# Optimization experiments

Hardware: AMD Instinct MI355X
Metric: run time of the kernel (lower is better)

The kernel has to match this reference:

```python
import jax, jax.numpy as jnp
import numpy as np
import math

N_STATE = 64
H_MODEL = 1024
D_CONV = 16
EXPAND = 2
D_INNER = EXPAND * H_MODEL            # 2048
HEADDIM = H_MODEL // 4                # 256
NHEADS = D_INNER // HEADDIM           # 8
NGROUPS = 1
CONV_DIM = D_INNER + 2 * NGROUPS * N_STATE           # 2176
D_IN_PROJ = 2 * D_INNER + 2 * NGROUPS * N_STATE + NHEADS
BATCH, SEQLEN = 4, 2048


def setup_inputs() -> dict:
    key = jax.random.key(0)
    ks = jax.random.split(key, 10)
    x = jax.random.normal(ks[0], (BATCH, SEQLEN, H_MODEL), jnp.float32)
    W_in = jax.random.normal(ks[1], (H_MODEL, D_IN_PROJ), jnp.float32) * (H_MODEL ** -0.5)
    conv_w = jax.random.normal(ks[2], (CONV_DIM, D_CONV), jnp.float32) * (D_CONV ** -0.5)
    conv_b = jnp.zeros((CONV_DIM,), jnp.float32)
    # inverse-softplus of dt0 in [1e-3, 1e-1] (mamba2 dt init)
    dt0 = jnp.exp(jax.random.uniform(ks[3], (NHEADS,), minval=math.log(1e-3), maxval=math.log(1e-1)))
    dt_bias = jnp.log(jnp.expm1(dt0))
    A_log = jnp.log(jax.random.uniform(ks[4], (NHEADS,), minval=1.0, maxval=16.0))
    D = jnp.ones((NHEADS,), jnp.float32)
    init_states = jax.random.normal(ks[5], (NHEADS, HEADDIM, N_STATE), jnp.float32) * 0.01
    norm_w = jnp.ones((D_INNER,), jnp.float32)
    W_out = jax.random.normal(ks[6], (D_INNER, H_MODEL), jnp.float32) * (D_INNER ** -0.5)
    W_nl = jax.random.normal(ks[7], (H_MODEL, H_MODEL), jnp.float32) * (H_MODEL ** -0.5)
    b_nl = jnp.zeros((H_MODEL,), jnp.float32)
    return dict(x=x, W_in=W_in, conv_w=conv_w, conv_b=conv_b, dt_bias=dt_bias,
                A_log=A_log, D=D, init_states=init_states, norm_w=norm_w,
                W_out=W_out, W_nl=W_nl, b_nl=b_nl)


def _mamba2(x, W_in, conv_w, conv_b, dt_bias, A_log, D, init_states, norm_w, W_out):
    b, l, _ = x.shape
    zxbcdt = x @ W_in                                  # (b, l, d_in_proj)
    z = zxbcdt[..., :D_INNER]
    xBC = zxbcdt[..., D_INNER:D_INNER + CONV_DIM]
    dt = jax.nn.softplus(zxbcdt[..., -NHEADS:] + dt_bias)   # (b, l, nheads)
    # depthwise causal conv1d (torch conv1d == cross-correlation)
    kernel = conv_w.T[:, None, :]                      # (K, 1, conv_dim)
    xBC = jax.lax.conv_general_dilated(
        xBC, kernel, window_strides=(1,), padding=[(D_CONV - 1, 0)],
        dimension_numbers=('NWC', 'WIO', 'NWC'), feature_group_count=CONV_DIM) + conv_b
    xBC = jax.nn.silu(xBC)
    xs = xBC[..., :D_INNER].reshape(b, l, NHEADS, HEADDIM)  # (b, l, h, p)
    Bm = xBC[..., D_INNER:D_INNER + N_STATE]                 # (b, l, n)
    Cm = xBC[..., D_INNER + N_STATE:]                        # (b, l, n)
    A = -jnp.exp(A_log)                                      # (nheads,) negative
    dA = jnp.exp(dt * A)                                     # (b, l, h)
    h0 = jnp.broadcast_to(init_states, (b, NHEADS, HEADDIM, N_STATE))

    def step(h, inp):
        dA_t, x_t, dt_t, B_t, C_t = inp
        dBx = jnp.einsum('bh,bhp,bn->bhpn', dt_t, x_t, B_t)
        h = h * dA_t[:, :, None, None] + dBx
        y_t = jnp.einsum('bhpn,bn->bhp', h, C_t)
        return h, y_t

    scan_in = (jnp.moveaxis(dA, 1, 0), jnp.moveaxis(xs, 1, 0), jnp.moveaxis(dt, 1, 0),
               jnp.moveaxis(Bm, 1, 0), jnp.moveaxis(Cm, 1, 0))
    _, ys = jax.lax.scan(step, h0, scan_in)
    y = jnp.moveaxis(ys, 0, 1) + D[None, None, :, None] * xs  # D skip connection
    y = y.reshape(b, l, D_INNER)
    # gated RMSNorm: rmsnorm(y * silu(z)) * norm_w, eps=1e-5
    y = y * jax.nn.silu(z)
    y = y * jax.lax.rsqrt(jnp.mean(y * y, axis=-1, keepdims=True) + 1e-5) * norm_w
    return y @ W_out


def reference(x, W_in, conv_w, conv_b, dt_bias, A_log, D, init_states, norm_w, W_out, W_nl, b_nl):
    y = _mamba2(x, W_in, conv_w, conv_b, dt_bias, A_log, D, init_states, norm_w, W_out)
    t = y / jnp.sqrt(1.0 + y * y)   # TanhApprox
    return t @ W_nl + b_nl + x      # Linear + residual
```

## Files before the change

### kernel.cpp

```cpp
#include <hip/hip_runtime.h>
#include <stdint.h>
#include <stddef.h>

#define BATCH   4
#define SEQLEN  2048
#define HM      1024
#define DINNER  2048
#define NH      8
#define HD      256
#define NS      64
#define CONVD   2176
#define DCONV   16
#define DPROJ   4232
#define ROWS    (BATCH*SEQLEN)
#define QC      256
#define NC      (SEQLEN/QC)
#define SC      64
#define TT      16

typedef __attribute__((ext_vector_type(8))) short short8;
typedef __attribute__((ext_vector_type(4))) short short4v;
typedef __attribute__((ext_vector_type(4))) float f32x4;

static constexpr size_t O_WOUT   = 0;
static constexpr size_t O_WNL    = 4194304;
static constexpr size_t O_DT     = 6291456;
static constexpr size_t O_LDA    = 6553600;
static constexpr size_t O_PG     = 6815744;
static constexpr size_t O_BT     = 6819840;
static constexpr size_t O_ZB     = 7868416;
static constexpr size_t O_XBCPRE = 41422848;
static constexpr size_t O_SG     = O_XBCPRE;
static constexpr size_t O_HG     = O_XBCPRE + 16777216;
static constexpr size_t O_TB     = O_XBCPRE;
static constexpr size_t O_XBC    = 77074432;
static constexpr size_t O_YN     = O_XBC;
static constexpr size_t O_XTR    = 112726016;
static constexpr size_t O_XBF    = O_XTR;
static constexpr size_t O_WIN    = O_XTR + 16777216;
static constexpr size_t O_WTAIL  = 146280448;

__device__ __forceinline__ short f2bf(float f) {
  union { float f; uint32_t u; } v; v.f = f;
  uint32_t r = v.u + 0x7fffu + ((v.u >> 16) & 1u);
  return (short)(r >> 16);
}

__device__ __forceinline__ float bf2f(short s) {
  union { float f; uint32_t u; } v;
  v.u = ((uint32_t)(uint16_t)s) << 16;
  return v.f;
}

__device__ __forceinline__ void gload_lds16(const void* g, void* l) {
  __builtin_amdgcn_global_load_lds(
      (const __attribute__((address_space(1))) uint32_t*)g,
      (__attribute__((address_space(3))) uint32_t*)l, 16, 0, 0);
}

__device__ __forceinline__ float sigmoidf_fast(float x) {
  return 1.f / (1.f + __expf(-x));
}

__device__ __forceinline__ short8 fragr(const char* base, int row, int kbyte) {
  return *(const short8*)(base + row * 128 + (kbyte ^ ((row & 7) << 4)));
}

__device__ __forceinline__ void transpose_tile(const float* __restrict__ W,
                                               short* __restrict__ Wt,
                                               int idx, int srcN, int validN,
                                               int Kdim, int nTilesN, int tid) {
  __shared__ short lds[64][72];
  int k0 = (idx / nTilesN) * 64;
  int n0 = (idx % nTilesN) * 64;
  int rr = tid >> 4;
  int cc = (tid & 15) * 4;
#pragma unroll
  for (int pass = 0; pass < 4; ++pass) {
    int k = pass * 16 + rr;
    int gn = n0 + cc;
    f32x4 v = (f32x4)0.f;
    if (gn < validN) v = *(const f32x4*)(W + (size_t)(k0 + k) * srcN + gn);
    uint32_t p0 = (uint32_t)(uint16_t)f2bf(v[0]) | ((uint32_t)(uint16_t)f2bf(v[1]) << 16);
    uint32_t p1 = (uint32_t)(uint16_t)f2bf(v[2]) | ((uint32_t)(uint16_t)f2bf(v[3]) << 16);
    *(uint32_t*)&lds[k][cc] = p0;
    *(uint32_t*)&lds[k][cc + 2] = p1;
  }
  __syncthreads();
  int n = tid >> 2;
  int ks = (tid & 3) * 16;
  short8 a, b;
#pragma unroll
  for (int j = 0; j < 8; ++j) a[j] = lds[ks + j][n];
#pragma unroll
  for (int j = 0; j < 8; ++j) b[j] = lds[ks + 8 + j][n];
  short* dst = Wt + (size_t)(n0 + n) * Kdim + k0 + ks;
  *(short8*)dst = a;
  *(short8*)(dst + 8) = b;
}

__global__ __launch_bounds__(256)
void prep_weights_kernel(const float* __restrict__ W_in, const float* __restrict__ W_out,
                         const float* __restrict__ W_nl,
                         short* __restrict__ winT, short* __restrict__ woutT,
                         short* __restrict__ wnlT, float* __restrict__ wtailT) {
  int bid = blockIdx.x, tid = threadIdx.x;
  if (bid < 1056) {
    transpose_tile(W_in, winT, bid, DPROJ, DPROJ, HM, 66, tid);
  } else if (bid < 1568) {
    transpose_tile(W_out, woutT, bid - 1056, HM, HM, DINNER, 16, tid);
  } else if (bid < 1824) {
    transpose_tile(W_nl, wnlT, bid - 1568, HM, HM, HM, 16, tid);
  } else {
    int i = (bid - 1824) * 256 + tid;
    int h = i >> 10, k = i & 1023;
    wtailT[i] = W_in[(size_t)k * DPROJ + (DPROJ - NH) + h];
  }
}

__global__ __launch_bounds__(256)
void cast_dt_kernel(const float* __restrict__ x, const float* __restrict__ wtailT,
                    const float* __restrict__ dt_bias, const float* __restrict__ A_log,
                    short* __restrict__ xbf, float* __restrict__ dtg,
                    float* __restrict__ ldA) {
  int row = blockIdx.x, tid = threadIdx.x;
  f32x4 xv = ((const f32x4*)(x + (size_t)row * HM))[tid];
  short4v o = { f2bf(xv[0]), f2bf(xv[1]), f2bf(xv[2]), f2bf(xv[3]) };
  ((short4v*)(xbf + (size_t)row * HM))[tid] = o;
  float p[NH];
#pragma unroll
  for (int h = 0; h < NH; ++h) {
    f32x4 w = ((const f32x4*)(wtailT + h * HM))[tid];
    p[h] = xv[0] * w[0] + xv[1] * w[1] + xv[2] * w[2] + xv[3] * w[3];
  }
#pragma unroll
  for (int h = 0; h < NH; ++h)
#pragma unroll
    for (int of = 32; of; of >>= 1) p[h] += __shfl_down(p[h], of);
  __shared__ float red[4][NH];
  int lane = tid & 63, w4 = tid >> 6;
  if (lane == 0)
#pragma unroll
    for (int h = 0; h < NH; ++h) red[w4][h] = p[h];
  __syncthreads();
  if (tid < NH) {
    float s = red[0][tid] + red[1][tid] + red[2][tid] + red[3][tid] + dt_bias[tid];
    float dtv = (s > 20.f) ? s : log1pf(expf(s));
    float A = -expf(A_log[tid]);
    dtg[row * NH + tid] = dtv;
    ldA[row * NH + tid] = dtv * A;
  }
}

__device__ __forceinline__ void prefix_aa(float av, float* aa, float* wsum,
                                          int tid) {
  float v = av;
  int lane = tid & 63;
#pragma unroll
  for (int o = 1; o < 64; o <<= 1) {
    float u = __shfl_up(v, o);
    if (lane >= o) v += u;
  }
  if (lane == 63) wsum[tid >> 6] = v;
  __syncthreads();
  float off = 0.f;
  int w4 = tid >> 6;
#pragma unroll
  for (int w = 0; w < 4; ++w)
    if (w < w4) off += wsum[w];
  aa[tid + 1] = v + off;
  if (tid == 0) aa[0] = 0.f;
  __syncthreads();
}

__global__ __launch_bounds__(512)
void gemm1_256(const short* __restrict__ A, const short* __restrict__ B,
               int K, int nTilesN,
               short* __restrict__ Cb, short* __restrict__ Cb2) {
  __shared__ alignas(16) char lds[49152];
  char* As = lds;
  char* Bs = lds + 32768;
  const int tid = threadIdx.x;
  int bid = blockIdx.x;
  {
    int nwg = gridDim.x;
    if ((nwg & 7) == 0) bid = (bid & 7) * (nwg >> 3) + (bid >> 3);
  }
  const int m0 = (bid / nTilesN) * 256;
  const int n0 = (bid % nTilesN) * 128;
  const int lane = tid & 63;
  const int wid = tid >> 6;
  const int wm = wid >> 1;
  const int wn = wid & 1;
  const int lrow = lane & 15, lk = lane >> 4;

  f32x4 acc[4][4];
#pragma unroll
  for (int i = 0; i < 4; ++i)
#pragma unroll
    for (int j = 0; j < 4; ++j) acc[i][j] = (f32x4)0.f;

  for (int k0 = 0; k0 < K; k0 += 64) {
#pragma unroll
    for (int r = 0; r < 4; ++r) {
      int p = r * 8192 + tid * 16;
      int row = p >> 7, c = p & 127;
      int sc = c ^ ((row & 7) << 4);
      gload_lds16((const char*)A + ((size_t)(m0 + row) * K + k0) * 2 + sc, As + p);
    }
#pragma unroll
    for (int r = 0; r < 2; ++r) {
      int p = r * 8192 + tid * 16;
      int row = p >> 7, c = p & 127;
      int sc = c ^ ((row & 7) << 4);
      gload_lds16((const char*)B + ((size_t)(n0 + row) * K + k0) * 2 + sc, Bs + p);
    }
    asm volatile("s_waitcnt vmcnt(0)" ::: "memory");
    __syncthreads();
#pragma unroll
    for (int ks = 0; ks < 2; ++ks) {
      short8 av[4], bv[4];
#pragma unroll
      for (int i = 0; i < 4; ++i) {
        av[i] = fragr(As, wm * 64 + i * 16 + lrow, ks * 64 + lk * 16);
        bv[i] = fragr(Bs, wn * 64 + i * 16 + lrow, ks * 64 + lk * 16);
      }
#pragma unroll
      for (int i = 0; i < 4; ++i)
#pragma unroll
        for (int j = 0; j < 4; ++j)
          acc[i][j] = __builtin_amdgcn_mfma_f32_16x16x32_bf16(av[i], bv[j], acc[i][j], 0, 0, 0);
    }
    __syncthreads();
  }

  const int row0 = m0 + wm * 64, col0 = n0 + wn * 64;
#pragma unroll
  for (int i = 0; i < 4; ++i)
#pragma unroll
    for (int j = 0; j < 4; ++j)
#pragma unroll
      for (int r = 0; r < 4; ++r) {
        int row = row0 + i * 16 + lk * 4 + r;
        int col = col0 + j * 16 + lrow;
        float v = acc[i][j][r];
        if (col < DINNER) Cb[(size_t)row * DINNER + col] = f2bf(v);
        else if (col < DINNER + CONVD) Cb2[(size_t)row * CONVD + (col - DINNER)] = f2bf(v);
      }
}

template <int EPI>
__global__ __launch_bounds__(512)
void gemm8p(const short* __restrict__ A, const short* __restrict__ B,
            int K, int nTilesN, int N_out,
            float* __restrict__ Cf, short* __restrict__ Cb,
            const float* __restrict__ bias, const float* __restrict__ resid) {
  __shared__ alignas(16) char lds[147456];
  const int tid = threadIdx.x;
  int bid = blockIdx.x;
  {
    int nwg = gridDim.x;
    if ((nwg & 7) == 0) bid = (bid & 7) * (nwg >> 3) + (bid >> 3);
  }
  const int m0 = (bid / nTilesN) * 256;
  const int n0 = (bid % nTilesN) * 128;
  const int lane = tid & 63;
  const int wid = tid >> 6;
  const int wm = wid >> 1;
  const int wn = wid & 1;
  const int lrow = lane & 15, lk = lane >> 4;
  const int nK = K >> 6;

#define LDSA(s) (lds + (s) * 49152)
#define LDSB(s) (lds + (s) * 49152 + 32768)

#define STAGE_A(s, kt, it) do {                                              \
    int p_ = (it) * 8192 + tid * 16;                                         \
    int row_ = p_ >> 7, c_ = p_ & 127;                                       \
    int sc_ = c_ ^ ((row_ & 7) << 4);                                        \
    gload_lds16((const char*)A + ((size_t)(m0 + row_) * K + (kt) * 64) * 2 + sc_, \
                LDSA(s) + p_);                                               \
  } while (0)
#define STAGE_B(s, kt, it) do {                                              \
    int p_ = (it) * 8192 + tid * 16;                                         \
    int row_ = p_ >> 7, c_ = p_ & 127;                                       \
    int sc_ = c_ ^ ((row_ & 7) << 4);                                        \
    gload_lds16((const char*)B + ((size_t)(n0 + row_) * K + (kt) * 64) * 2 + sc_, \
                LDSB(s) + p_);                                               \
  } while (0)

  f32x4 acc[4][4];
#pragma unroll
  for (int i = 0; i < 4; ++i)
#pragma unroll
    for (int j = 0; j < 4; ++j) acc[i][j] = (f32x4)0.f;

#pragma unroll
  for (int it = 0; it < 4; ++it) STAGE_A(0, 0, it);
#pragma unroll
  for (int it = 0; it < 2; ++it) STAGE_B(0, 0, it);
#pragma unroll
  for (int it = 0; it < 4; ++it) STAGE_A(1, 1, it);
#pragma unroll
  for (int it = 0; it < 2; ++it) STAGE_B(1, 1, it);
  asm volatile("s_waitcnt vmcnt(6)" ::: "memory");
  __builtin_amdgcn_s_barrier();

  for (int kt = 0; kt < nK; ++kt) {
    const int rs = kt % 3;
    const int ss = (kt + 2) % 3;
    const bool st = (kt + 2) < nK;
    const char* Ab = LDSA(rs);
    const char* Bb = LDSB(rs);
    short8 aF[4][2], bF[4][2];

#pragma unroll
    for (int ii = 0; ii < 4; ++ii)
#pragma unroll
      for (int ks = 0; ks < 2; ++ks)
        aF[ii][ks] = fragr(Ab, wm * 64 + ii * 16 + lrow, ks * 64 + lk * 16);
#pragma unroll
    for (int jj = 0; jj < 2; ++jj)
#pragma unroll
      for (int ks = 0; ks < 2; ++ks)
        bF[jj][ks] = fragr(Bb, wn * 64 + jj * 16 + lrow, ks * 64 + lk * 16);
    if (st) { STAGE_A(ss, kt + 2, 0); STAGE_A(ss, kt + 2, 1); STAGE_A(ss, kt + 2, 2); STAGE_A(ss, kt + 2, 3); }
    __builtin_amdgcn_s_barrier();
    asm volatile("s_waitcnt lgkmcnt(0)" ::: "memory");
    __builtin_amdgcn_s_setprio(1);
#pragma unroll
    for (int ii = 0; ii < 4; ++ii)
#pragma unroll
      for (int jj = 0; jj < 2; ++jj)
#pragma unroll
        for (int ks = 0; ks < 2; ++ks)
          acc[ii][jj] = __builtin_amdgcn_mfma_f32_16x16x32_bf16(aF[ii][ks], bF[jj][ks], acc[ii][jj], 0, 0, 0);
    __builtin_amdgcn_s_setprio(0);
    __builtin_amdgcn_s_barrier();

#pragma unroll
    for (int jj = 2; jj < 4; ++jj)
#pragma unroll
      for (int ks = 0; ks < 2; ++ks)
        bF[jj][ks] = fragr(Bb, wn * 64 + jj * 16 + lrow, ks * 64 + lk * 16);
    if (st) { STAGE_B(ss, kt + 2, 0); STAGE_B(ss, kt + 2, 1); }
    __builtin_amdgcn_s_barrier();
    asm volatile("s_waitcnt lgkmcnt(0)" ::: "memory");
    __builtin_amdgcn_s_setprio(1);
#pragma unroll
    for (int ii = 0; ii < 4; ++ii)
#pragma unroll
      for (int jj = 2; jj < 4; ++jj)
#pragma unroll
        for (int ks = 0; ks < 2; ++ks)
          acc[ii][jj] = __builtin_amdgcn_mfma_f32_16x16x32_bf16(aF[ii][ks], bF[jj][ks], acc[ii][jj], 0, 0, 0);
    __builtin_amdgcn_s_setprio(0);
    if (kt >= nK - 2) {
      asm volatile("s_waitcnt vmcnt(0)" ::: "memory");
    } else {
      asm volatile("s_waitcnt vmcnt(6)" ::: "memory");
    }
    __builtin_amdgcn_s_barrier();
  }

  const int row0 = m0 + wm * 64, col0 = n0 + wn * 64;
#pragma unroll
  for (int i = 0; i < 4; ++i)
#pragma unroll
    for (int j = 0; j < 4; ++j)
#pragma unroll
      for (int r = 0; r < 4; ++r) {
        int row = row0 + i * 16 + lk * 4 + r;
        int col = col0 + j * 16 + lrow;
        float v = acc[i][j][r];
        if (EPI == 1) {
          float t = v * rsqrtf(1.f + v * v);
          Cb[(size_t)row * N_out + col] = f2bf(t);
        } else if (EPI == 2) {
          Cf[(size_t)row * N_out + col] = v + bias[col] + resid[(size_t)row * N_out + col];
        }
      }
#undef LDSA
#undef LDSB
#undef STAGE_A
#undef STAGE_B
}

__global__ __launch_bounds__(256) void conv_silu_kernel(const short* __restrict__ xbcpre,
                                                        const float* __restrict__ cw,
                                                        const float* __restrict__ cbias,
                                                        short* __restrict__ bc,
                                                        short* __restrict__ xT,
                                                        short* __restrict__ bTg) {
  __shared__ short tld[64][130];
  int blk = blockIdx.x;
  int cg = blk % 17;
  int tg = (blk / 17) % 32;
  int b  = blk / (17 * 32);
  int lane = threadIdx.x & 63;
  int warp = threadIdx.x >> 6;
  int c0 = cg * 128 + lane * 2;
  int tbase = (tg * 4 + warp) * TT;

  const short* inp = xbcpre + (size_t)(b * SEQLEN) * CONVD + c0;
  uint32_t in[TT + DCONV - 1];
#pragma unroll
  for (int j = 0; j < TT + DCONV - 1; ++j) {
    int t = tbase + j - (DCONV - 1);
    in[j] = (t >= 0) ? *(const uint32_t*)(inp + (size_t)t * CONVD) : 0u;
  }
  float w0[DCONV], w1[DCONV];
  const float* wp = cw + (size_t)c0 * DCONV;
#pragma unroll
  for (int k = 0; k < DCONV; ++k) { w0[k] = wp[k]; w1[k] = wp[DCONV + k]; }
  float bb0 = cbias[c0], bb1 = cbias[c0 + 1];

  const bool isBC = (cg == 16);
  short* bcp = bc + (size_t)(b * SEQLEN) * 128 + (c0 - DINNER);
#pragma unroll
  for (int tt = 0; tt < TT; ++tt) {
    float a0 = bb0, a1 = bb1;
#pragma unroll
    for (int k = 0; k < DCONV; ++k) {
      uint32_t v = in[tt + k];
      a0 = fmaf(bf2f((short)(v & 0xffffu)), w0[k], a0);
      a1 = fmaf(bf2f((short)(v >> 16)), w1[k], a1);
    }
    a0 = a0 * sigmoidf_fast(a0);
    a1 = a1 * sigmoidf_fast(a1);
    uint32_t o = (uint32_t)(uint16_t)f2bf(a0) | ((uint32_t)(uint16_t)f2bf(a1) << 16);
    if (isBC) *(uint32_t*)(bcp + (size_t)(tbase + tt) * 128) = o;
    *(uint32_t*)&tld[warp * TT + tt][lane * 2] = o;
  }
  __syncthreads();
  int ch = threadIdx.x & 127;
  int seg = threadIdx.x >> 7;
  int gc = cg * 128 + ch;
  short* dst = nullptr;
  if (gc < DINNER) dst = xT + (size_t)gc * ROWS;
  else if (gc < DINNER + NS) dst = bTg + (size_t)(gc - DINNER) * ROWS;
  if (dst) {
    int tcol = b * SEQLEN + tg * 64 + seg * 32;
    short8 v[4];
#pragma unroll
    for (int q = 0; q < 4; ++q)
#pragma unroll
      for (int j = 0; j < 8; ++j) v[q][j] = tld[seg * 32 + q * 8 + j][ch];
    short8* dp = (short8*)(dst + tcol);
    dp[0] = v[0]; dp[1] = v[1]; dp[2] = v[2]; dp[3] = v[3];
  }
}

__global__ __launch_bounds__(256)
void scan_passA_mfma(const short* __restrict__ xT, const short* __restrict__ bTg,
                     const float* __restrict__ dtg, const float* __restrict__ ldA,
                     float* __restrict__ Sg, float* __restrict__ Pg) {
  __shared__ alignas(16) char Ax[32768];
  __shared__ alignas(16) char Bt[8192];
  __shared__ float aa[QC + 1];
  __shared__ float wdt[QC];
  __shared__ float wsum[4];
  int blk = blockIdx.x;
  int c8 = blk & 7, bh = blk >> 3;
  int h = bh & 7, b = bh >> 3;
  int tid = threadIdx.x, wave = tid >> 6, lane = tid & 63;
  int lrow = lane & 15, lk = lane >> 4;
  int rowbase = b * SEQLEN + c8 * QC;
  prefix_aa(ldA[(rowbase + tid) * NH + h], aa, wsum, tid);
  float alast = aa[QC];
  if (tid == 0) Pg[blk] = __expf(alast);
  wdt[tid] = __expf(alast - aa[tid + 1]) * dtg[(rowbase + tid) * NH + h];

  f32x4 acc[4][4];
#pragma unroll
  for (int i = 0; i < 4; ++i)
#pragma unroll
    for (int j = 0; j < 4; ++j) acc[i][j] = (f32x4)0.f;

  for (int ks = 0; ks < 4; ++ks) {
    int s0 = ks * 64;
#pragma unroll
    for (int it = 0; it < 8; ++it) {
      int p = it * 4096 + tid * 16;
      int row = p >> 7, c = p & 127;
      int sc = c ^ ((row & 7) << 4);
      gload_lds16((const char*)(xT + (size_t)(h * HD + row) * ROWS + rowbase + s0) + sc, Ax + p);
    }
#pragma unroll
    for (int it = 0; it < 2; ++it) {
      int p = it * 4096 + tid * 16;
      int row = p >> 7, c = p & 127;
      int sc = c ^ ((row & 7) << 4);
      gload_lds16((const char*)(bTg + (size_t)row * ROWS + rowbase + s0) + sc, Bt + p);
    }
    asm volatile("s_waitcnt vmcnt(0)" ::: "memory");
    __syncthreads();
    {
      int row = tid;
#pragma unroll
      for (int g = 0; g < 8; ++g) {
        int off = row * 128 + g * 16;
        int sb = s0 + (((g * 16) ^ ((row & 7) << 4)) >> 1);
        short8 v = *(short8*)(Ax + off);
        short8 o;
#pragma unroll
        for (int j = 0; j < 8; ++j) o[j] = f2bf(bf2f(v[j]) * wdt[sb + j]);
        *(short8*)(Ax + off) = o;
      }
    }
    __syncthreads();
#pragma unroll
    for (int kk = 0; kk < 2; ++kk) {
      short8 av[4], bv[4];
#pragma unroll
      for (int i = 0; i < 4; ++i) {
        av[i] = fragr(Ax, wave * 64 + i * 16 + lrow, kk * 64 + lk * 16);
        bv[i] = fragr(Bt, i * 16 + lrow, kk * 64 + lk * 16);
      }
#pragma unroll
      for (int i = 0; i < 4; ++i)
#pragma unroll
        for (int j = 0; j < 4; ++j)
          acc[i][j] = __builtin_amdgcn_mfma_f32_16x16x32_bf16(av[i], bv[j], acc[i][j], 0, 0, 0);
    }
    __syncthreads();
  }
#pragma unroll
  for (int i = 0; i < 4; ++i)
#pragma unroll
    for (int j = 0; j < 4; ++j)
#pragma unroll
      for (int r = 0; r < 4; ++r) {
        int p = wave * 64 + i * 16 + lk * 4 + r;
        int n = j * 16 + lrow;
        Sg[((size_t)blk * 256 + p) * 64 + n] = acc[i][j][r];
      }
}

__global__ __launch_bounds__(256)
void scan_passB(const float* __restrict__ Sg, const float* __restrict__ Pg,
                const float* __restrict__ init, float* __restrict__ Hg) {
  int blk = blockIdx.x;
  int ptile = blk & 15, bh = blk >> 4;
  int h = bh & (NH - 1);
  int tid = threadIdx.x;
  size_t off = (size_t)ptile * 1024 + tid * 4;
  f32x4 hc = *(const f32x4*)(init + (size_t)h * HD * NS + off);
#pragma unroll 1
  for (int c = 0; c < NC; ++c) {
    *(f32x4*)(Hg + (size_t)(bh * NC + c) * 16384 + off) = hc;
    float P = Pg[bh * NC + c];
    f32x4 s = *(const f32x4*)(Sg + (size_t)(bh * NC + c) * 16384 + off);
    hc = P * hc + s;
  }
}

__global__ __launch_bounds__(256)
void scan_passC_mfma(const short* __restrict__ xT, const short* __restrict__ bTg,
                     const short* __restrict__ bc,
                     const float* __restrict__ dtg, const float* __restrict__ ldA,
                     const float* __restrict__ Hg, const float* __restrict__ Dp,
                     short* __restrict__ yfull) {
  __shared__ alignas(16) char Xb[32768];
  __shared__ alignas(16) char Hb[32768];
  __shared__ alignas(16) char Bn[8192];
  __shared__ alignas(16) char Cn[8192];
  __shared__ alignas(16) char Bt2[8192];
  __shared__ alignas(16) char Mm[8192];
  __shared__ float aa[QC + 1];
  __shared__ float dts[QC];
  __shared__ float wsum[4];
  int blk = blockIdx.x;
  int c8 = blk & 7, bh = blk >> 3;
  int h = bh & 7, b = bh >> 3;
  int tid = threadIdx.x, wave = tid >> 6, lane = tid & 63;
  int lrow = lane & 15, lk = lane >> 4;
  int rowbase = b * SEQLEN + c8 * QC;
  prefix_aa(ldA[(rowbase + tid) * NH + h], aa, wsum, tid);
  dts[tid] = dtg[(rowbase + tid) * NH + h];
  __syncthreads();
  float Dh = Dp[h];

  f32x4 hcc[4][4];
  const float* hp = Hg + (size_t)blk * 16384;
#pragma unroll
  for (int i = 0; i < 4; ++i)
#pragma unroll
    for (int j = 0; j < 4; ++j)
#pragma unroll
      for (int r = 0; r < 4; ++r)
        hcc[i][j][r] = hp[(size_t)(wave * 64 + i * 16 + lk * 4 + r) * 64 + j * 16 + lrow];

  for (int sc = 0; sc < 4; ++sc) {
    int s0 = sc * SC;
#pragma unroll
    for (int i = 0; i < 4; ++i)
#pragma unroll
      for (int j = 0; j < 4; ++j)
#pragma unroll
        for (int r = 0; r < 4; ++r) {
          int p = wave * 64 + i * 16 + lk * 4 + r;
          int n = j * 16 + lrow;
          *(short*)(Hb + p * 128 + ((n * 2) ^ ((p & 7) << 4))) = f2bf(hcc[i][j][r]);
        }
#pragma unroll
    for (int it = 0; it < 8; ++it) {
      int p = it * 4096 + tid * 16;
      int row = p >> 7, c = p & 127;
      int scz = c ^ ((row & 7) << 4);
      gload_lds16((const char*)(xT + (size_t)(h * HD + row) * ROWS + rowbase + s0) + scz, Xb + p);
    }
#pragma unroll
    for (int it = 0; it < 2; ++it) {
      int p = it * 4096 + tid * 16;
      int row = p >> 7, c = p & 127;
      int scz = c ^ ((row & 7) << 4);
      gload_lds16((const char*)(bc + (size_t)(rowbase + s0 + row) * 128) + scz, Bn + p);
      gload_lds16((const char*)(bc + (size_t)(rowbase + s0 + row) * 128 + NS) + scz, Cn + p);
      gload_lds16((const char*)(bTg + (size_t)row * ROWS + rowbase + s0) + scz, Bt2 + p);
    }
    asm volatile("s_waitcnt vmcnt(0)" ::: "memory");
    __syncthreads();

    f32x4 gcc[4];
#pragma unroll
    for (int j = 0; j < 4; ++j) gcc[j] = (f32x4)0.f;
#pragma unroll
    for (int kk = 0; kk < 2; ++kk) {
      short8 avc = fragr(Cn, wave * 16 + lrow, kk * 64 + lk * 16);
#pragma unroll
      for (int j = 0; j < 4; ++j) {
        short8 bvb = fragr(Bn, j * 16 + lrow, kk * 64 + lk * 16);
        gcc[j] = __builtin_amdgcn_mfma_f32_16x16x32_bf16(avc, bvb, gcc[j], 0, 0, 0);
      }
    }
#pragma unroll
    for (int j = 0; j < 4; ++j)
#pragma unroll
      for (int r = 0; r < 4; ++r) {
        int t = wave * 16 + lk * 4 + r;
        int s = j * 16 + lrow;
        float val = (s <= t) ? gcc[j][r] * __expf(aa[s0 + t + 1] - aa[s0 + s + 1]) * dts[s0 + s]
                             : 0.f;
        *(short*)(Mm + t * 128 + ((s * 2) ^ ((t & 7) << 4))) = f2bf(val);
      }
#pragma unroll
    for (int pass = 0; pass < 2; ++pass) {
      int t = wave * 16 + (lane >> 3) + pass * 8;
      int g = lane & 7;
      int off = t * 128 + g * 16;
      float fac = __expf(aa[s0 + t + 1] - aa[s0]);
      short8 v = *(short8*)(Cn + off);
      short8 o;
#pragma unroll
      for (int j = 0; j < 8; ++j) o[j] = f2bf(bf2f(v[j]) * fac);
      *(short8*)(Cn + off) = o;
    }
    __syncthreads();

    f32x4 ycc[4][4];
#pragma unroll
    for (int i = 0; i < 4; ++i)
#pragma unroll
      for (int j = 0; j < 4; ++j) ycc[i][j] = (f32x4)0.f;
#pragma unroll
    for (int kk = 0; kk < 2; ++kk) {
      short8 av[4], bv[4];
#pragma unroll
      for (int i = 0; i < 4; ++i) {
        av[i] = fragr(Mm, i * 16 + lrow, kk * 64 + lk * 16);
        bv[i] = fragr(Xb, wave * 64 + i * 16 + lrow, kk * 64 + lk * 16);
      }
#pragma unroll
      for (int i = 0; i < 4; ++i)
#pragma unroll
        for (int j = 0; j < 4; ++j)
          ycc[i][j] = __builtin_amdgcn_mfma_f32_16x16x32_bf16(av[i], bv[j], ycc[i][j], 0, 0, 0);
    }
#pragma unroll
    for (int kk = 0; kk < 2; ++kk) {
      short8 av[4], bv[4];
#pragma unroll
      for (int i = 0; i < 4; ++i) {
        av[i] = fragr(Cn, i * 16 + lrow, kk * 64 + lk * 16);
        bv[i] = fragr(Hb, wave * 64 + i * 16 + lrow, kk * 64 + lk * 16);
      }
#pragma unroll
      for (int i = 0; i < 4; ++i)
#pragma unroll
        for (int j = 0; j < 4; ++j)
          ycc[i][j] = __builtin_amdgcn_mfma_f32_16x16x32_bf16(av[i], bv[j], ycc[i][j], 0, 0, 0);
    }
#pragma unroll
    for (int i = 0; i < 4; ++i)
#pragma unroll
      for (int j = 0; j < 4; ++j)
#pragma unroll
        for (int r = 0; r < 4; ++r) {
          int t = i * 16 + lk * 4 + r;
          int p = wave * 64 + j * 16 + lrow;
          float xv = bf2f(*(const short*)(Xb + p * 128 + ((t * 2) ^ ((p & 7) << 4))));
          yfull[(size_t)(rowbase + s0 + t) * DINNER + h * HD + p] = f2bf(ycc[i][j][r] + Dh * xv);
        }
    {
      int row = tid;
      float aend = aa[s0 + SC];
#pragma unroll
      for (int g = 0; g < 8; ++g) {
        int off = row * 128 + g * 16;
        int sb = s0 + (((g * 16) ^ ((row & 7) << 4)) >> 1);
        short8 v = *(short8*)(Xb + off);
        short8 o;
#pragma unroll
        for (int j = 0; j < 8; ++j)
          o[j] = f2bf(bf2f(v[j]) * __expf(aend - aa[sb + j + 1]) * dts[sb + j]);
        *(short8*)(Xb + off) = o;
      }
    }
    {
      float Ps = __expf(aa[s0 + SC] - aa[s0]);
#pragma unroll
      for (int i = 0; i < 4; ++i)
#pragma unroll
        for (int j = 0; j < 4; ++j) hcc[i][j] *= Ps;
#pragma unroll
      for (int kk = 0; kk < 2; ++kk) {
        short8 av[4], bv[4];
#pragma unroll
        for (int i = 0; i < 4; ++i) {
          av[i] = fragr(Xb, wave * 64 + i * 16 + lrow, kk * 64 + lk * 16);
          bv[i] = fragr(Bt2, i * 16 + lrow, kk * 64 + lk * 16);
        }
#pragma unroll
        for (int i = 0; i < 4; ++i)
#pragma unroll
          for (int j = 0; j < 4; ++j)
            hcc[i][j] = __builtin_amdgcn_mfma_f32_16x16x32_bf16(av[i], bv[j], hcc[i][j], 0, 0, 0);
      }
    }
    __syncthreads();
  }
}

__global__ __launch_bounds__(256)
void gate_norm_kernel(const short* __restrict__ yfull, const short* __restrict__ zb,
                      const float* __restrict__ norm_w, short* __restrict__ yn) {
  int row = blockIdx.x, tid = threadIdx.x;
  size_t yb = (size_t)row * DINNER;
  float v[8];
  float ss = 0.f;
#pragma unroll
  for (int g = 0; g < 2; ++g) {
    int cidx = g * 1024 + tid * 4;
    short4v y4 = *(const short4v*)(yfull + yb + cidx);
    short4v z4 = *(const short4v*)(zb + yb + cidx);
#pragma unroll
    for (int j = 0; j < 4; ++j) {
      float z = bf2f(z4[j]);
      float val = bf2f(y4[j]) * z * sigmoidf_fast(z);
      v[g * 4 + j] = val;
      ss = fmaf(val, val, ss);
    }
  }
#pragma unroll
  for (int o = 32; o; o >>= 1) ss += __shfl_down(ss, o);
  __shared__ float red[4];
  if ((tid & 63) == 0) red[tid >> 6] = ss;
  __syncthreads();
  float tot = red[0] + red[1] + red[2] + red[3];
  float scale = rsqrtf(tot * (1.f / (float)DINNER) + 1e-5f);
#pragma unroll
  for (int g = 0; g < 2; ++g) {
    int cidx = g * 1024 + tid * 4;
    short4v o4;
#pragma unroll
    for (int j = 0; j < 4; ++j) o4[j] = f2bf(v[g * 4 + j] * scale * norm_w[cidx + j]);
    *(short4v*)(yn + yb + cidx) = o4;
  }
}

extern "C" void kernel_launch(void* const* d_in, const int* in_sizes, int n_in,
                              void* d_out, int out_size, void* d_ws, size_t ws_size,
                              hipStream_t stream) {
  (void)in_sizes; (void)n_in; (void)out_size; (void)ws_size;
  const float* x     = (const float*)d_in[0];
  const float* W_in  = (const float*)d_in[1];
  const float* convw = (const float*)d_in[2];
  const float* convb = (const float*)d_in[3];
  const float* dtb   = (const float*)d_in[4];
  const float* Alog  = (const float*)d_in[5];
  const float* Dp    = (const float*)d_in[6];
  const float* inis  = (const float*)d_in[7];
  const float* nw    = (const float*)d_in[8];
  const float* W_out = (const float*)d_in[9];
  const float* W_nl  = (const float*)d_in[10];
  const float* b_nl  = (const float*)d_in[11];
  float* out = (float*)d_out;
  char* ws = (char*)d_ws;

  short* woutT  = (short*)(ws + O_WOUT);
  short* wnlT   = (short*)(ws + O_WNL);
  float* dtg    = (float*)(ws + O_DT);
  float* ldA    = (float*)(ws + O_LDA);
  float* Pg     = (float*)(ws + O_PG);
  short* bTg    = (short*)(ws + O_BT);
  short* zb     = (short*)(ws + O_ZB);
  short* xbcpre = (short*)(ws + O_XBCPRE);
  float* Sg     = (float*)(ws + O_SG);
  float* Hg     = (float*)(ws + O_HG);
  short* tb     = (short*)(ws + O_TB);
  short* bc     = (short*)(ws + O_XBC);
  short* yn     = (short*)(ws + O_YN);
  short* xT     = (short*)(ws + O_XTR);
  short* xbf    = (short*)(ws + O_XBF);
  short* winT   = (short*)(ws + O_WIN);
  float* wtailT = (float*)(ws + O_WTAIL);
  short* yfull  = (short*)d_out;

  prep_weights_kernel<<<1856, 256, 0, stream>>>(W_in, W_out, W_nl, winT, woutT, wnlT, wtailT);
  cast_dt_kernel<<<ROWS, 256, 0, stream>>>(x, wtailT, dtb, Alog, xbf, dtg, ldA);

  gemm1_256<<<32 * 33, 512, 0, stream>>>(xbf, winT, HM, 33, zb, xbcpre);
  conv_silu_kernel<<<17 * 32 * 4, 256, 0, stream>>>(xbcpre, convw, convb, bc, xT, bTg);

  scan_passA_mfma<<<32 * NC, 256, 0, stream>>>(xT, bTg, dtg, ldA, Sg, Pg);
  scan_passB<<<32 * 16, 256, 0, stream>>>(Sg, Pg, inis, Hg);
  scan_passC_mfma<<<32 * NC, 256, 0, stream>>>(xT, bTg, bc, dtg, ldA, Hg, Dp, yfull);

  gate_norm_kernel<<<ROWS, 256, 0, stream>>>(yfull, zb, nw, yn);
  gemm8p<1><<<32 * 8, 512, 0, stream>>>(yn, woutT, DINNER, 8, HM, nullptr, tb, nullptr, nullptr);
  gemm8p<2><<<32 * 8, 512, 0, stream>>>(tb, wnlT, HM, 8, HM, out, nullptr, b_nl, x);
}
```

Before: 323.7 us.

## Split scan passes A and C across headdim halves to double block count

Scan pass A and pass C now launch twice as many blocks, each handling 128 of the 256 headdim rows for a (batch, head, chunk). This halves LDS and accumulator registers per block and raises parallelism from 256 blocks to 512 on a GPU with many CUs. The cost is redundant work: each half recomputes the prefix sums, the intra-chunk C·B mask matrix, and loads B/C tiles twice.

```diff
diff --git a/kernel.cpp b/kernel.cpp
--- a/kernel.cpp
+++ b/kernel.cpp
@@ -455,36 +455,38 @@
 void scan_passA_mfma(const short* __restrict__ xT, const short* __restrict__ bTg,
                      const float* __restrict__ dtg, const float* __restrict__ ldA,
                      float* __restrict__ Sg, float* __restrict__ Pg) {
-  __shared__ alignas(16) char Ax[32768];
+  __shared__ alignas(16) char Ax[16384];
   __shared__ alignas(16) char Bt[8192];
   __shared__ float aa[QC + 1];
   __shared__ float wdt[QC];
   __shared__ float wsum[4];
-  int blk = blockIdx.x;
+  int blk2 = blockIdx.x;
+  int half = blk2 & 1, blk = blk2 >> 1;
   int c8 = blk & 7, bh = blk >> 3;
   int h = bh & 7, b = bh >> 3;
+  int pbase = half * 128;
   int tid = threadIdx.x, wave = tid >> 6, lane = tid & 63;
   int lrow = lane & 15, lk = lane >> 4;
   int rowbase = b * SEQLEN + c8 * QC;
   prefix_aa(ldA[(rowbase + tid) * NH + h], aa, wsum, tid);
   float alast = aa[QC];
-  if (tid == 0) Pg[blk] = __expf(alast);
+  if (tid == 0 && half == 0) Pg[blk] = __expf(alast);
   wdt[tid] = __expf(alast - aa[tid + 1]) * dtg[(rowbase + tid) * NH + h];
 
-  f32x4 acc[4][4];
-#pragma unroll
-  for (int i = 0; i < 4; ++i)
+  f32x4 acc[2][4];
+#pragma unroll
+  for (int i = 0; i < 2; ++i)
 #pragma unroll
     for (int j = 0; j < 4; ++j) acc[i][j] = (f32x4)0.f;
 
   for (int ks = 0; ks < 4; ++ks) {
     int s0 = ks * 64;
 #pragma unroll
-    for (int it = 0; it < 8; ++it) {
+    for (int it = 0; it < 4; ++it) {
       int p = it * 4096 + tid * 16;
       int row = p >> 7, c = p & 127;
       int sc = c ^ ((row & 7) << 4);
-      gload_lds16((const char*)(xT + (size_t)(h * HD + row) * ROWS + rowbase + s0) + sc, Ax + p);
+      gload_lds16((const char*)(xT + (size_t)(h * HD + pbase + row) * ROWS + rowbase + s0) + sc, Ax + p);
     }
 #pragma unroll
     for (int it = 0; it < 2; ++it) {
@@ -496,9 +498,11 @@
     asm volatile("s_waitcnt vmcnt(0)" ::: "memory");
     __syncthreads();
     {
-      int row = tid;
-#pragma unroll
-      for (int g = 0; g < 8; ++g) {
+      int row = wave * 32 + (lane & 31);
+      int gb = (lane >> 5) * 4;
+#pragma unroll
+      for (int gi = 0; gi < 4; ++gi) {
+        int g = gb + gi;
         int off = row * 128 + g * 16;
         int sb = s0 + (((g * 16) ^ ((row & 7) << 4)) >> 1);
         short8 v = *(short8*)(Ax + off);
@@ -511,14 +515,15 @@
     __syncthreads();
 #pragma unroll
     for (int kk = 0; kk < 2; ++kk) {
-      short8 av[4], bv[4];
-#pragma unroll
-      for (int i = 0; i < 4; ++i) {
-        av[i] = fragr(Ax, wave * 64 + i * 16 + lrow, kk * 64 + lk * 16);
-        bv[i] = fragr(Bt, i * 16 + lrow, kk * 64 + lk * 16);
-      }
-#pragma unroll
-      for (int i = 0; i < 4; ++i)
+      short8 av[2], bv[4];
+#pragma unroll
+      for (int i = 0; i < 2; ++i)
+        av[i] = fragr(Ax, wave * 32 + i * 16 + lrow, kk * 64 + lk * 16);
+#pragma unroll
+      for (int j = 0; j < 4; ++j)
+        bv[j] = fragr(Bt, j * 16 + lrow, kk * 64 + lk * 16);
+#pragma unroll
+      for (int i = 0; i < 2; ++i)
 #pragma unroll
         for (int j = 0; j < 4; ++j)
           acc[i][j] = __builtin_amdgcn_mfma_f32_16x16x32_bf16(av[i], bv[j], acc[i][j], 0, 0, 0);
@@ -526,12 +531,12 @@
     __syncthreads();
   }
 #pragma unroll
-  for (int i = 0; i < 4; ++i)
+  for (int i = 0; i < 2; ++i)
 #pragma unroll
     for (int j = 0; j < 4; ++j)
 #pragma unroll
       for (int r = 0; r < 4; ++r) {
-        int p = wave * 64 + i * 16 + lk * 4 + r;
+        int p = pbase + wave * 32 + i * 16 + lk * 4 + r;
         int n = j * 16 + lrow;
         Sg[((size_t)blk * 256 + p) * 64 + n] = acc[i][j][r];
       }
@@ -561,8 +566,8 @@
                      const float* __restrict__ dtg, const float* __restrict__ ldA,
                      const float* __restrict__ Hg, const float* __restrict__ Dp,
                      short* __restrict__ yfull) {
-  __shared__ alignas(16) char Xb[32768];
-  __shared__ alignas(16) char Hb[32768];
+  __shared__ alignas(16) char Xb[16384];
+  __shared__ alignas(16) char Hb[16384];
   __shared__ alignas(16) char Bn[8192];
   __shared__ alignas(16) char Cn[8192];
   __shared__ alignas(16) char Bt2[8192];
@@ -570,9 +575,11 @@
   __shared__ float aa[QC + 1];
   __shared__ float dts[QC];
   __shared__ float wsum[4];
-  int blk = blockIdx.x;
+  int blk2 = blockIdx.x;
+  int half = blk2 & 1, blk = blk2 >> 1;
   int c8 = blk & 7, bh = blk >> 3;
   int h = bh & 7, b = bh >> 3;
+  int pbase = half * 128;
   int tid = threadIdx.x, wave = tid >> 6, lane = tid & 63;
   int lrow = lane & 15, lk = lane >> 4;
   int rowbase = b * SEQLEN + c8 * QC;
@@ -581,34 +588,34 @@
   __syncthreads();
   float Dh = Dp[h];
 
-  f32x4 hcc[4][4];
+  f32x4 hcc[2][4];
   const float* hp = Hg + (size_t)blk * 16384;
 #pragma unroll
-  for (int i = 0; i < 4; ++i)
+  for (int i = 0; i < 2; ++i)
 #pragma unroll
     for (int j = 0; j < 4; ++j)
 #pragma unroll
       for (int r = 0; r < 4; ++r)
-        hcc[i][j][r] = hp[(size_t)(wave * 64 + i * 16 + lk * 4 + r) * 64 + j * 16 + lrow];
+        hcc[i][j][r] = hp[(size_t)(pbase + wave * 32 + i * 16 + lk * 4 + r) * 64 + j * 16 + lrow];
 
   for (int sc = 0; sc < 4; ++sc) {
     int s0 = sc * SC;
 #pragma unroll
-    for (int i = 0; i < 4; ++i)
+    for (int i = 0; i < 2; ++i)
 #pragma unroll
       for (int j = 0; j < 4; ++j)
 #pragma unroll
         for (int r = 0; r < 4; ++r) {
-          int p = wave * 64 + i * 16 + lk * 4 + r;
+          int pl = wave * 32 + i * 16 + lk * 4 + r;
           int n = j * 16 + lrow;
-          *(short*)(Hb + p * 128 + ((n * 2) ^ ((p & 7) << 4))) = f2bf(hcc[i][j][r]);
+          *(short*)(Hb + pl * 128 + ((n * 2) ^ ((pl & 7) << 4))) = f2bf(hcc[i][j][r]);
         }
 #pragma unroll
-    for (int it = 0; it < 8; ++it) {
+    for (int it = 0; it < 4; ++it) {
       int p = it * 4096 + tid * 16;
       int row = p >> 7, c = p & 127;
       int scz = c ^ ((row & 7) << 4);
-      gload_lds16((const char*)(xT + (size_t)(h * HD + row) * ROWS + rowbase + s0) + scz, Xb + p);
+      gload_lds16((const char*)(xT + (size_t)(h * HD + pbase + row) * ROWS + rowbase + s0) + scz, Xb + p);
     }
 #pragma unroll
     for (int it = 0; it < 2; ++it) {
@@ -658,55 +665,59 @@
     }
     __syncthreads();
 
-    f32x4 ycc[4][4];
+    f32x4 ycc[4][2];
 #pragma unroll
     for (int i = 0; i < 4; ++i)
 #pragma unroll
-      for (int j = 0; j < 4; ++j) ycc[i][j] = (f32x4)0.f;
+      for (int j = 0; j < 2; ++j) ycc[i][j] = (f32x4)0.f;
 #pragma unroll
     for (int kk = 0; kk < 2; ++kk) {
-      short8 av[4], bv[4];
-#pragma unroll
-      for (int i = 0; i < 4; ++i) {
+      short8 av[4], bv[2];
+#pragma unroll
+      for (int i = 0; i < 4; ++i)
         av[i] = fragr(Mm, i * 16 + lrow, kk * 64 + lk * 16);
-        bv[i] = fragr(Xb, wave * 64 + i * 16 + lrow, kk * 64 + lk * 16);
-      }
+#pragma unroll
+      for (int j = 0; j < 2; ++j)
+        bv[j] = fragr(Xb, wave * 32 + j * 16 + lrow, kk * 64 + lk * 16);
 #pragma unroll
       for (int i = 0; i < 4; ++i)
 #pragma unroll
-        for (int j = 0; j < 4; ++j)
+        for (int j = 0; j < 2; ++j)
           ycc[i][j] = __builtin_amdgcn_mfma_f32_16x16x32_bf16(av[i], bv[j], ycc[i][j], 0, 0, 0);
     }
 #pragma unroll
     for (int kk = 0; kk < 2; ++kk) {
-      short8 av[4], bv[4];
-#pragma unroll
-      for (int i = 0; i < 4; ++i) {
+      short8 av[4], bv[2];
+#pragma unroll
+      for (int i = 0; i < 4; ++i)
         av[i] = fragr(Cn, i * 16 + lrow, kk * 64 + lk * 16);
-        bv[i] = fragr(Hb, wave * 64 + i * 16 + lrow, kk * 64 + lk * 16);
-      }
+#pragma unroll
+      for (int j = 0; j < 2; ++j)
+        bv[j] = fragr(Hb, wave * 32 + j * 16 + lrow, kk * 64 + lk * 16);
 #pragma unroll
       for (int i = 0; i < 4; ++i)
 #pragma unroll
-        for (int j = 0; j < 4; ++j)
+        for (int j = 0; j < 2; ++j)
           ycc[i][j] = __builtin_amdgcn_mfma_f32_16x16x32_bf16(av[i], bv[j], ycc[i][j], 0, 0, 0);
     }
 #pragma unroll
     for (int i = 0; i < 4; ++i)
 #pragma unroll
-      for (int j = 0; j < 4; ++j)
+      for (int j = 0; j < 2; ++j)
 #pragma unroll
         for (int r = 0; r < 4; ++r) {
           int t = i * 16 + lk * 4 + r;
-          int p = wave * 64 + j * 16 + lrow;
-          float xv = bf2f(*(const short*)(Xb + p * 128 + ((t * 2) ^ ((p & 7) << 4))));
-          yfull[(size_t)(rowbase + s0 + t) * DINNER + h * HD + p] = f2bf(ycc[i][j][r] + Dh * xv);
+          int pl = wave * 32 + j * 16 + lrow;
+          float xv = bf2f(*(const short*)(Xb + pl * 128 + ((t * 2) ^ ((pl & 7) << 4))));
+          yfull[(size_t)(rowbase + s0 + t) * DINNER + h * HD + pbase + pl] = f2bf(ycc[i][j][r] + Dh * xv);
         }
     {
-      int row = tid;
+      int row = wave * 32 + (lane & 31);
+      int gb = (lane >> 5) * 4;
       float aend = aa[s0 + SC];
 #pragma unroll
-      for (int g = 0; g < 8; ++g) {
+      for (int gi = 0; gi < 4; ++gi) {
+        int g = gb + gi;
         int off = row * 128 + g * 16;
         int sb = s0 + (((g * 16) ^ ((row & 7) << 4)) >> 1);
         short8 v = *(short8*)(Xb + off);
@@ -720,19 +731,20 @@
     {
       float Ps = __expf(aa[s0 + SC] - aa[s0]);
 #pragma unroll
-      for (int i = 0; i < 4; ++i)
+      for (int i = 0; i < 2; ++i)
 #pragma unroll
         for (int j = 0; j < 4; ++j) hcc[i][j] *= Ps;
 #pragma unroll
       for (int kk = 0; kk < 2; ++kk) {
-        short8 av[4], bv[4];
-#pragma unroll
-        for (int i = 0; i < 4; ++i) {
-          av[i] = fragr(Xb, wave * 64 + i * 16 + lrow, kk * 64 + lk * 16);
-          bv[i] = fragr(Bt2, i * 16 + lrow, kk * 64 + lk * 16);
-        }
-#pragma unroll
-        for (int i = 0; i < 4; ++i)
+        short8 av[2], bv[4];
+#pragma unroll
+        for (int i = 0; i < 2; ++i)
+          av[i] = fragr(Xb, wave * 32 + i * 16 + lrow, kk * 64 + lk * 16);
+#pragma unroll
+        for (int j = 0; j < 4; ++j)
+          bv[j] = fragr(Bt2, j * 16 + lrow, kk * 64 + lk * 16);
+#pragma unroll
+        for (int i = 0; i < 2; ++i)
 #pragma unroll
           for (int j = 0; j < 4; ++j)
             hcc[i][j] = __builtin_amdgcn_mfma_f32_16x16x32_bf16(av[i], bv[j], hcc[i][j], 0, 0, 0);
@@ -823,9 +835,9 @@
   gemm1_256<<<32 * 33, 512, 0, stream>>>(xbf, winT, HM, 33, zb, xbcpre);
   conv_silu_kernel<<<17 * 32 * 4, 256, 0, stream>>>(xbcpre, convw, convb, bc, xT, bTg);
 
-  scan_passA_mfma<<<32 * NC, 256, 0, stream>>>(xT, bTg, dtg, ldA, Sg, Pg);
+  scan_passA_mfma<<<32 * NC * 2, 256, 0, stream>>>(xT, bTg, dtg, ldA, Sg, Pg);
   scan_passB<<<32 * 16, 256, 0, stream>>>(Sg, Pg, inis, Hg);
-  scan_passC_mfma<<<32 * NC, 256, 0, stream>>>(xT, bTg, bc, dtg, ldA, Hg, Dp, yfull);
+  scan_passC_mfma<<<32 * NC * 2, 256, 0, stream>>>(xT, bTg, bc, dtg, ldA, Hg, Dp, yfull);
 
   gate_norm_kernel<<<ROWS, 256, 0, stream>>>(yfull, zb, nw, yn);
   gemm8p<1><<<32 * 8, 512, 0, stream>>>(yn, woutT, DINNER, 8, HM, nullptr, tb, nullptr, nullptr);
```

Result: faster. 289.9 us (median of 2 runs) (-10.5%).
